# Performance work log

Measured on AMD Instinct MI355X. Metric: run time of the kernel, lower is better.

Reference implementation:

```python
import jax, jax.numpy as jnp
import numpy as np
import math

NUM_BINS, NUM_FREQS, NUM_KERNELS, MLP_HIDDEN = 128, 64, 3, 64
NUM_KEYS = 8192
ANCHORS = jnp.array([1000.0, 10000.0, 100000.0], dtype=jnp.float32)
LOG_ANCHORS = jnp.log10(ANCHORS)


def setup_inputs() -> dict:
    key = jax.random.key(0)
    ks = jax.random.split(key, 12)
    K = jax.random.normal(ks[0], (NUM_KEYS, 2 * NUM_FREQS), dtype=jnp.float32)
    key_positions = jax.random.randint(ks[1], (NUM_KEYS,), 0, 131072, dtype=jnp.int32)
    reference_angles = jax.random.normal(ks[2], (NUM_FREQS,), dtype=jnp.float32)
    # KernelEncodingLayer params
    centers = jnp.array([2 * math.pi * m / NUM_KERNELS - math.pi for m in range(NUM_KERNELS)], dtype=jnp.float32)
    mu = jax.random.normal(ks[3], (NUM_BINS, NUM_FREQS, NUM_KERNELS), dtype=jnp.float32) * 0.1 + centers
    kappa = jnp.ones((NUM_BINS, NUM_FREQS, NUM_KERNELS), dtype=jnp.float32)
    weight = jax.random.normal(ks[4], (NUM_BINS, NUM_FREQS, NUM_KERNELS), dtype=jnp.float32) * 0.1
    bias = jnp.zeros((NUM_BINS,), dtype=jnp.float32)
    # MLP params (kaiming-uniform-ish init)
    lim1 = 1.0 / math.sqrt(NUM_BINS)
    W1 = jax.random.uniform(ks[5], (MLP_HIDDEN, NUM_BINS), jnp.float32, -lim1, lim1)
    b1 = jax.random.uniform(ks[6], (MLP_HIDDEN,), jnp.float32, -lim1, lim1)
    lim2 = 1.0 / math.sqrt(MLP_HIDDEN)
    W2 = jax.random.uniform(ks[7], (1, MLP_HIDDEN), jnp.float32, -lim2, lim2)
    b2 = jax.random.uniform(ks[8], (1,), jnp.float32, -lim2, lim2)
    # PositionScalingLayer: softplus^-1(1.0)
    anchor_raw = jnp.full((3,), math.log(math.exp(1.0) - 1), dtype=jnp.float32)
    return {"K": K, "key_positions": key_positions, "reference_angles": reference_angles,
            "mu": mu, "kappa": kappa, "weight": weight, "bias": bias,
            "W1": W1, "b1": b1, "W2": W2, "b2": b2, "anchor_raw": anchor_raw}


def _position_weights(positions, anchor_raw):
    aw = jax.nn.softplus(anchor_raw)  # (3,)
    log_pos = jnp.log10(jnp.maximum(positions.astype(jnp.float32), 1.0))  # (N,)
    w = jnp.full_like(log_pos, aw[0])
    for i in range(LOG_ANCHORS.shape[0] - 1):
        ll, lr = LOG_ANCHORS[i], LOG_ANCHORS[i + 1]
        t = (log_pos - ll) / (lr - ll)
        interp = aw[i] * (1 - t) + aw[i + 1] * t
        w = jnp.where((log_pos >= ll) & (log_pos < lr), interp, w)
    w = jnp.where(log_pos >= LOG_ANCHORS[-1], aw[-1], w)
    return w


def reference(K, key_positions, reference_angles, mu, kappa, weight, bias, W1, b1, W2, b2, anchor_raw):
    N = K.shape[0]
    Kc = K.reshape(N, NUM_FREQS, 2)            # (N, F, 2)
    magnitude = jnp.linalg.norm(Kc, axis=2)     # (N, F)
    angle = jnp.arctan2(Kc[..., 1], Kc[..., 0])  # (N, F)
    mu_eff = mu + reference_angles[None, :, None]  # (B, F, M)
    # von Mises kernel: (N, B, F, M)
    kern = jnp.exp(kappa[None] * (jnp.cos(angle[:, None, :, None] - mu_eff[None]) - 1.0))
    wk = jnp.einsum('nbfm,bfm->nbf', kern, weight)       # sum over kernels
    logits = jnp.einsum('nbf,nf->nb', wk, magnitude) + bias  # (N, B)
    h = jax.nn.relu(logits @ W1.T + b1)
    mlp_out = (h @ W2.T + b2)[:, 0]            # (N,)
    pos_w = _position_weights(key_positions, anchor_raw)
    return jax.nn.sigmoid(mlp_out * pos_w)
```

## Files before the change

kernel.cpp:

```cpp
#include <hip/hip_runtime.h>
#include <math.h>

#define NBINS 128
#define NFREQ 64
#define NH    4
#define NSEG  (2*NH+1)
#define KDIM  (NSEG*NFREQ)
#define KSTEPS (KDIM/32)
#define ROWF  (KDIM+8)
#define ROWL  (NBINS+8)
#define ROWP  68

typedef _Float16 f16x8 __attribute__((ext_vector_type(8)));
typedef _Float16 f16x2 __attribute__((ext_vector_type(2)));
typedef float    f32x4 __attribute__((ext_vector_type(4)));

#define MFMA16(A,B,C) __builtin_amdgcn_mfma_f32_16x16x32_f16((A),(B),(C),0,0,0)

__global__ __launch_bounds__(192) void prep_kernel(
    const float* __restrict__ mu, const float* __restrict__ kappa,
    const float* __restrict__ weight, const float* __restrict__ ref,
    const float* __restrict__ W1,
    _Float16* __restrict__ Cfrag, _Float16* __restrict__ W1h)
{
    __shared__ float red[3][64][10];

    const int t = threadIdx.x;
    const int m = t >> 6;
    const int g = t & 63;
    const int G = blockIdx.x * 64 + g;
    const int f = G & 63;

    int wid = blockIdx.x * 192 + t;
    if (wid < NBINS * 64) W1h[wid] = (_Float16)W1[wid];

    const int idx = G * 3 + m;
    float kap = kappa[idx];
    float wgt = weight[idx];
    float mue = mu[idx] + ref[f];

    float I[NH + 1];
    {
        const float rfact[NH + 1] = {1.f, 1.f, 0.5f, 1.f / 6.f, 1.f / 24.f};
        float x2 = kap * 0.5f, x2sq = x2 * x2;
        float xk = 1.f;
        #pragma unroll
        for (int k = 0; k <= NH; ++k) {
            if (k > 0) xk *= x2;
            float term = xk * rfact[k];
            float s = term;
            #pragma unroll
            for (int j = 1; j <= 12; ++j) {
                term *= x2sq * (1.f / ((float)j * (float)(j + k)));
                s += term;
            }
            I[k] = s;
        }
    }
    float e = expf(-kap) * wgt;
    float c1, s1; sincosf(mue, &s1, &c1);
    float ck = 1.f, sk = 0.f;
    red[m][g][0] = e * I[0];
    #pragma unroll
    for (int k = 1; k <= NH; ++k) {
        float cn = ck * c1 - sk * s1;
        float sn = sk * c1 + ck * s1;
        ck = cn; sk = sn;
        red[m][g][2 * k - 1] = e * 2.f * I[k] * ck;
        red[m][g][2 * k]     = e * 2.f * I[k] * sk;
    }
    __syncthreads();

    if (t < 64) {
        int G2 = blockIdx.x * 64 + t;
        int bin = G2 >> 6, ff = G2 & 63, bt = bin >> 4;
        #pragma unroll
        for (int seg = 0; seg < NSEG; ++seg) {
            float v = red[0][t][seg] + red[1][t][seg] + red[2][t][seg];
            int q = seg * NFREQ + ff;
            int ks = q >> 5, kk = q & 31;
            int lane = (bin & 15) | (((kk >> 3) & 3) << 4);
            int elem = kk & 7;
            Cfrag[((size_t)(ks * 8 + bt) * 64 + lane) * 8 + elem] = (_Float16)v;
        }
    }
}

__global__ __launch_bounds__(256) void main_kernel(
    const float* __restrict__ K, const int* __restrict__ kpos,
    const float* __restrict__ bias, const float* __restrict__ b1,
    const float* __restrict__ W2, const float* __restrict__ b2,
    const float* __restrict__ anchor_raw,
    const _Float16* __restrict__ Cfrag, const _Float16* __restrict__ W1h,
    float* __restrict__ out)
{
    __shared__ _Float16 PhiF[16 * ROWF];
    __shared__ _Float16 LgF[16 * ROWL];
    __shared__ float    Ps[16 * ROWP];
    __shared__ float    Pr[256];

    const int t  = threadIdx.x;
    const int n0 = blockIdx.x * 16;

    #pragma unroll
    for (int it = 0; it < 2; ++it) {
        int p = it * 256 + t;
        int key = p >> 5, f2 = p & 31;
        float4 xy = *(const float4*)(K + (size_t)(n0 + key) * 128 + f2 * 4);
        float vs[2][NSEG];
        #pragma unroll
        for (int e = 0; e < 2; ++e) {
            float x = e ? xy.z : xy.x;
            float y = e ? xy.w : xy.y;
            float r2 = x * x + y * y;
            float inv = r2 > 0.f ? rsqrtf(r2) : 0.f;
            vs[e][0] = r2 * inv;
            float ca = x * inv, sa = y * inv;
            float mc = x, ms = y;
            vs[e][1] = mc; vs[e][2] = ms;
            #pragma unroll
            for (int h = 2; h <= NH; ++h) {
                float mc2 = mc * ca - ms * sa;
                float ms2 = ms * ca + mc * sa;
                mc = mc2; ms = ms2;
                vs[e][2 * h - 1] = mc; vs[e][2 * h] = ms;
            }
        }
        _Float16* dst = PhiF + key * ROWF + 2 * f2;
        #pragma unroll
        for (int s = 0; s < NSEG; ++s) {
            f16x2 pk; pk.x = (_Float16)vs[0][s]; pk.y = (_Float16)vs[1][s];
            *(f16x2*)(dst + s * 64) = pk;
        }
    }
    __syncthreads();

    const int l = t & 63, w = t >> 6;
    f32x4 acc[2] = {};
    const _Float16* phA = PhiF + (l & 15) * ROWF + (l >> 4) * 8;
    const _Float16* cb  = Cfrag + (size_t)(2 * w) * 512 + (size_t)l * 8;
    #define LA(KS) (*(const f16x8*)(phA + (KS) * 32))
    #define LB(KS, BT) (*(const f16x8*)(cb + ((size_t)(KS) * 8 + (BT)) * 512))

    f16x8 b00 = LB(0, 0), b01 = LB(0, 1), b10 = LB(1, 0), b11 = LB(1, 1);
    f16x8 a0 = LA(0);
    #pragma unroll
    for (int ks = 0; ks < KSTEPS; ++ks) {
        int kb = ks + 2 < KSTEPS ? ks + 2 : KSTEPS - 1;
        f16x8 nb0 = LB(kb, 0), nb1 = LB(kb, 1);
        int ka = ks + 1 < KSTEPS ? ks + 1 : KSTEPS - 1;
        f16x8 na0 = LA(ka);
        acc[0] = MFMA16(a0, b00, acc[0]);
        acc[1] = MFMA16(a0, b01, acc[1]);
        a0 = na0;
        b00 = b10; b01 = b11; b10 = nb0; b11 = nb1;
    }
    #undef LA
    #undef LB

    #pragma unroll
    for (int bt = 0; bt < 2; ++bt) {
        int bin = 32 * w + bt * 16 + (l & 15);
        float bbv = bias[bin];
        #pragma unroll
        for (int r = 0; r < 4; ++r) {
            int key = (l >> 4) * 4 + r;
            LgF[key * ROWL + bin] = (_Float16)(acc[bt][r] + bbv);
        }
    }
    __syncthreads();

    f32x4 hacc = {};
    const _Float16* lgA = LgF + (l & 15) * ROWL + (l >> 4) * 8;
    const _Float16* wb  = W1h + (size_t)(16 * w + (l & 15)) * 128 + (l >> 4) * 8;
    #pragma unroll
    for (int ks = 0; ks < 4; ++ks) {
        f16x8 bfr = *(const f16x8*)(wb + ks * 32);
        f16x8 am  = *(const f16x8*)(lgA + ks * 32);
        hacc = MFMA16(am, bfr, hacc);
    }
    {
        int j = 16 * w + (l & 15);
        float b1j = b1[j], w2j = W2[j];
        #pragma unroll
        for (int r = 0; r < 4; ++r) {
            int key = (l >> 4) * 4 + r;
            float h = hacc[r] + b1j;
            Ps[key * ROWP + j] = fmaxf(h, 0.f) * w2j;
        }
    }
    __syncthreads();

    {
        int key = t >> 4, gg = t & 15;
        const float* p = Ps + key * ROWP + gg * 4;
        Pr[t] = (p[0] + p[1]) + (p[2] + p[3]);
    }
    __syncthreads();
    if (t < 16) {
        const float* p = Pr + t * 16;
        float s = (((p[0] + p[1]) + (p[2] + p[3])) + ((p[4] + p[5]) + (p[6] + p[7])))
                + (((p[8] + p[9]) + (p[10] + p[11])) + ((p[12] + p[13]) + (p[14] + p[15])));
        float mlp = s + b2[0];
        float aw0 = log1pf(expf(anchor_raw[0]));
        float aw1 = log1pf(expf(anchor_raw[1]));
        float aw2 = log1pf(expf(anchor_raw[2]));
        int n = n0 + t;
        float pf = (float)kpos[n];
        float lp = log10f(fmaxf(pf, 1.f));
        float wgt;
        if      (lp < 3.f) wgt = aw0;
        else if (lp < 4.f) wgt = fmaf(aw1 - aw0, lp - 3.f, aw0);
        else if (lp < 5.f) wgt = fmaf(aw2 - aw1, lp - 4.f, aw1);
        else               wgt = aw2;
        float z = mlp * wgt;
        out[n] = 1.f / (1.f + expf(-z));
    }
}

extern "C" void kernel_launch(void* const* d_in, const int* in_sizes, int n_in,
                              void* d_out, int out_size, void* d_ws, size_t ws_size,
                              hipStream_t stream)
{
    const float* K    = (const float*)d_in[0];
    const int*   kpos = (const int*)d_in[1];
    const float* ref  = (const float*)d_in[2];
    const float* mu   = (const float*)d_in[3];
    const float* kap  = (const float*)d_in[4];
    const float* wgt  = (const float*)d_in[5];
    const float* bias = (const float*)d_in[6];
    const float* W1   = (const float*)d_in[7];
    const float* b1   = (const float*)d_in[8];
    const float* W2   = (const float*)d_in[9];
    const float* b2   = (const float*)d_in[10];
    const float* anc  = (const float*)d_in[11];
    float* out = (float*)d_out;

    int N = in_sizes[0] / (2 * NFREQ);

    char* ws = (char*)d_ws;
    _Float16* Cfrag = (_Float16*)ws;
    _Float16* W1h   = (_Float16*)(ws + 147456);

    prep_kernel<<<128, 192, 0, stream>>>(mu, kap, wgt, ref, W1, Cfrag, W1h);
    main_kernel<<<N / 16, 256, 0, stream>>>(K, kpos, bias, b1, W2, b2, anc,
                                            Cfrag, W1h, out);
}
```

Before: 86.22 us.

## Process 32 keys per block with 8 waves and reuse B fragments across two M-tiles

The main kernel now handles 32 keys per block using 512 threads. Each of the 8 waves owns one 16-bin tile and applies every loaded Cfrag B fragment to two 16-key A tiles, which halves global B traffic per key and halves the block count. The MLP stage is remapped so each wave computes one 16x16 tile of hidden units. The Bessel series in the prep kernel is also shortened from 12 to 6 terms, which cuts prep arithmetic but may lose some accuracy for larger kappa values.

```diff
diff --git a/kernel.cpp b/kernel.cpp
--- a/kernel.cpp
+++ b/kernel.cpp
@@ -10,6 +10,7 @@
 #define ROWF  (KDIM+8)
 #define ROWL  (NBINS+8)
 #define ROWP  68
+#define MKEYS 32
 
 typedef _Float16 f16x8 __attribute__((ext_vector_type(8)));
 typedef _Float16 f16x2 __attribute__((ext_vector_type(2)));
@@ -50,7 +51,7 @@
             float term = xk * rfact[k];
             float s = term;
             #pragma unroll
-            for (int j = 1; j <= 12; ++j) {
+            for (int j = 1; j <= 6; ++j) {
                 term *= x2sq * (1.f / ((float)j * (float)(j + k)));
                 s += term;
             }
@@ -86,7 +87,7 @@
     }
 }
 
-__global__ __launch_bounds__(256) void main_kernel(
+__global__ __launch_bounds__(512, 2) void main_kernel(
     const float* __restrict__ K, const int* __restrict__ kpos,
     const float* __restrict__ bias, const float* __restrict__ b1,
     const float* __restrict__ W2, const float* __restrict__ b2,
@@ -94,17 +95,17 @@
     const _Float16* __restrict__ Cfrag, const _Float16* __restrict__ W1h,
     float* __restrict__ out)
 {
-    __shared__ _Float16 PhiF[16 * ROWF];
-    __shared__ _Float16 LgF[16 * ROWL];
-    __shared__ float    Ps[16 * ROWP];
-    __shared__ float    Pr[256];
+    __shared__ _Float16 PhiF[MKEYS * ROWF];
+    __shared__ _Float16 LgF[MKEYS * ROWL];
+    __shared__ float    Ps[MKEYS * ROWP];
+    __shared__ float    Pr[512];
 
     const int t  = threadIdx.x;
-    const int n0 = blockIdx.x * 16;
+    const int n0 = blockIdx.x * MKEYS;
 
     #pragma unroll
     for (int it = 0; it < 2; ++it) {
-        int p = it * 256 + t;
+        int p = it * 512 + t;
         int key = p >> 5, f2 = p & 31;
         float4 xy = *(const float4*)(K + (size_t)(n0 + key) * 128 + f2 * 4);
         float vs[2][NSEG];
@@ -138,53 +139,56 @@
     const int l = t & 63, w = t >> 6;
     f32x4 acc[2] = {};
     const _Float16* phA = PhiF + (l & 15) * ROWF + (l >> 4) * 8;
-    const _Float16* cb  = Cfrag + (size_t)(2 * w) * 512 + (size_t)l * 8;
-    #define LA(KS) (*(const f16x8*)(phA + (KS) * 32))
-    #define LB(KS, BT) (*(const f16x8*)(cb + ((size_t)(KS) * 8 + (BT)) * 512))
-
-    f16x8 b00 = LB(0, 0), b01 = LB(0, 1), b10 = LB(1, 0), b11 = LB(1, 1);
-    f16x8 a0 = LA(0);
+    const _Float16* cb  = Cfrag + ((size_t)w * 64 + l) * 8;
+    #define LA(KS, MT) (*(const f16x8*)(phA + (MT) * 16 * ROWF + (KS) * 32))
+    #define LB(KS)     (*(const f16x8*)(cb + (size_t)(KS) * 4096))
+
+    f16x8 b0 = LB(0), b1f = LB(1);
+    f16x8 a0 = LA(0, 0), a1 = LA(0, 1);
     #pragma unroll
     for (int ks = 0; ks < KSTEPS; ++ks) {
         int kb = ks + 2 < KSTEPS ? ks + 2 : KSTEPS - 1;
-        f16x8 nb0 = LB(kb, 0), nb1 = LB(kb, 1);
+        f16x8 nb = LB(kb);
         int ka = ks + 1 < KSTEPS ? ks + 1 : KSTEPS - 1;
-        f16x8 na0 = LA(ka);
-        acc[0] = MFMA16(a0, b00, acc[0]);
-        acc[1] = MFMA16(a0, b01, acc[1]);
-        a0 = na0;
-        b00 = b10; b01 = b11; b10 = nb0; b11 = nb1;
+        f16x8 na0 = LA(ka, 0), na1 = LA(ka, 1);
+        acc[0] = MFMA16(a0, b0, acc[0]);
+        acc[1] = MFMA16(a1, b0, acc[1]);
+        a0 = na0; a1 = na1;
+        b0 = b1f; b1f = nb;
     }
     #undef LA
     #undef LB
 
-    #pragma unroll
-    for (int bt = 0; bt < 2; ++bt) {
-        int bin = 32 * w + bt * 16 + (l & 15);
+    {
+        int bin = 16 * w + (l & 15);
         float bbv = bias[bin];
         #pragma unroll
+        for (int mt = 0; mt < 2; ++mt) {
+            #pragma unroll
+            for (int r = 0; r < 4; ++r) {
+                int key = mt * 16 + (l >> 4) * 4 + r;
+                LgF[key * ROWL + bin] = (_Float16)(acc[mt][r] + bbv);
+            }
+        }
+    }
+    __syncthreads();
+
+    f32x4 hacc = {};
+    {
+        const int mt = w >> 2, jq = w & 3;
+        const int j  = jq * 16 + (l & 15);
+        const _Float16* lgA = LgF + (mt * 16 + (l & 15)) * ROWL + (l >> 4) * 8;
+        const _Float16* wb  = W1h + (size_t)j * 128 + (l >> 4) * 8;
+        #pragma unroll
+        for (int ks = 0; ks < 4; ++ks) {
+            f16x8 bfr = *(const f16x8*)(wb + ks * 32);
+            f16x8 am  = *(const f16x8*)(lgA + ks * 32);
+            hacc = MFMA16(am, bfr, hacc);
+        }
+        float b1j = b1[j], w2j = W2[j];
+        #pragma unroll
         for (int r = 0; r < 4; ++r) {
-            int key = (l >> 4) * 4 + r;
-            LgF[key * ROWL + bin] = (_Float16)(acc[bt][r] + bbv);
-        }
-    }
-    __syncthreads();
-
-    f32x4 hacc = {};
-    const _Float16* lgA = LgF + (l & 15) * ROWL + (l >> 4) * 8;
-    const _Float16* wb  = W1h + (size_t)(16 * w + (l & 15)) * 128 + (l >> 4) * 8;
-    #pragma unroll
-    for (int ks = 0; ks < 4; ++ks) {
-        f16x8 bfr = *(const f16x8*)(wb + ks * 32);
-        f16x8 am  = *(const f16x8*)(lgA + ks * 32);
-        hacc = MFMA16(am, bfr, hacc);
-    }
-    {
-        int j = 16 * w + (l & 15);
-        float b1j = b1[j], w2j = W2[j];
-        #pragma unroll
-        for (int r = 0; r < 4; ++r) {
-            int key = (l >> 4) * 4 + r;
+            int key = mt * 16 + (l >> 4) * 4 + r;
             float h = hacc[r] + b1j;
             Ps[key * ROWP + j] = fmaxf(h, 0.f) * w2j;
         }
@@ -197,7 +201,7 @@
         Pr[t] = (p[0] + p[1]) + (p[2] + p[3]);
     }
     __syncthreads();
-    if (t < 16) {
+    if (t < MKEYS) {
         const float* p = Pr + t * 16;
         float s = (((p[0] + p[1]) + (p[2] + p[3])) + ((p[4] + p[5]) + (p[6] + p[7])))
                 + (((p[8] + p[9]) + (p[10] + p[11])) + ((p[12] + p[13]) + (p[14] + p[15])));
@@ -243,6 +247,6 @@
     _Float16* W1h   = (_Float16*)(ws + 147456);
 
     prep_kernel<<<128, 192, 0, stream>>>(mu, kap, wgt, ref, W1, Cfrag, W1h);
-    main_kernel<<<N / 16, 256, 0, stream>>>(K, kpos, bias, b1, W2, b2, anc,
-                                            Cfrag, W1h, out);
+    main_kernel<<<N / MKEYS, 512, 0, stream>>>(K, kpos, bias, b1, W2, b2, anc,
+                                               Cfrag, W1h, out);
 }
```

New measurement: 85.98 us. Within noise of the previous version (-0.3%).
